# Optimization experiments

Measured on AMD Instinct MI355X. Metric: run time of the kernel, lower is better.

Reference implementation:

```python
import jax, jax.numpy as jnp
import numpy as np

B, T, DMODEL = 2, 2048, 1024
H, DK, DV = 16, 64, 64
FF = 4096
EPS = 1e-5


def _layernorm_2d(x):
    # torch LayerNorm(normalized_shape=(T, dmodel)): normalize jointly over last two
    # dims, biased variance, weight=1 / bias=0 (freshly constructed each forward).
    mu = jnp.mean(x, axis=(1, 2), keepdims=True)
    var = jnp.mean((x - mu) ** 2, axis=(1, 2), keepdims=True)
    return (x - mu) / jnp.sqrt(var + EPS)


def setup_inputs() -> dict:
    key = jax.random.key(0)
    ks = jax.random.split(key, 9)
    s = 0.02  # small init for numerical sanity (original uses uniform(-1,1))
    return {
        "x": jax.random.normal(ks[0], (B, T, DMODEL), jnp.float32),
        "Wq": jax.random.normal(ks[1], (H, DMODEL, DK), jnp.float32) * s,
        "Wk": jax.random.normal(ks[2], (H, DMODEL, DK), jnp.float32) * s,
        "Wv": jax.random.normal(ks[3], (H, DMODEL, DV), jnp.float32) * s,
        "Wo": jax.random.normal(ks[4], (DMODEL, DMODEL), jnp.float32) * s,
        "W1": jax.random.normal(ks[5], (DMODEL, FF), jnp.float32) * s,
        "b1": jnp.zeros((FF,), jnp.float32),
        "W2": jax.random.normal(ks[6], (FF, DMODEL), jnp.float32) * s,
        "b2": jnp.zeros((DMODEL,), jnp.float32),
    }


def reference(x, Wq, Wk, Wv, Wo, W1, b1, W2, b2):
    b, t, d = x.shape
    h, _, dk = Wq.shape
    dv = Wv.shape[-1]
    # per-head projections: (B,H,T,dk/dv)
    Qp = jnp.einsum("btd,hdk->bhtk", x, Wq)
    Kp = jnp.einsum("btd,hdk->bhtk", x, Wk)
    Vp = jnp.einsum("btd,hdv->bhtv", x, Wv)
    scores = jnp.einsum("bhqk,bhsk->bhqs", Qp, Kp) / np.sqrt(dk).astype(np.float32)
    # NOTE: original does torch.softmax(heads, 2) -> softmax over the QUERY axis
    attn = jax.nn.softmax(scores, axis=2)
    heads = jnp.einsum("bhqs,bhsv->bqhv", attn, Vp).reshape(b, t, h * dv)
    att_out = heads @ Wo
    o1 = _layernorm_2d(x + att_out)
    ff = jnp.maximum(o1 @ W1 + b1, 0.0) @ W2 + b2
    return _layernorm_2d(o1 + ff)
```

## Files before the change

kernel.cpp:

```cpp
#include <hip/hip_runtime.h>
#include <hip/hip_bf16.h>
#include <cstddef>
#include <cstdint>

typedef __hip_bfloat16 hbf;
typedef __attribute__((ext_vector_type(8))) __bf16 bf16x8;
typedef __attribute__((ext_vector_type(4))) float f32x4;

#define B_ 2
#define T_ 2048
#define D_ 1024
#define H_ 16
#define FF_ 4096
#define EPS_ 1e-5f
#define SCALE_ 0.18033688011112f

__device__ __forceinline__ float bf2f(hbf v) { return __bfloat162float(v); }
__device__ __forceinline__ float fexp2(float x) {
  return __builtin_amdgcn_exp2f(x);
}
__device__ __forceinline__ float flog2(float x) {
  return __builtin_amdgcn_logf(x);
}
__device__ __forceinline__ float ldin(const void* p, size_t i, int isbf) {
  return isbf ? __bfloat162float(((const hbf*)p)[i]) : ((const float*)p)[i];
}
__device__ __forceinline__ void ston(void* p, size_t i, float v, int isbf) {
  if (isbf) ((hbf*)p)[i] = __float2bfloat16(v);
  else ((float*)p)[i] = v;
}
__device__ __forceinline__ f32x4 mfma16(bf16x8 a, bf16x8 b, f32x4 c) {
  return __builtin_amdgcn_mfma_f32_16x16x32_bf16(a, b, c, 0, 0, 0);
}
__device__ __forceinline__ bf16x8 ldfrag(const hbf* p) {
  return *(const bf16x8*)p;
}
__device__ __forceinline__ void glds16(const hbf* g, hbf* l) {
  __builtin_amdgcn_global_load_lds(
      (const __attribute__((address_space(1))) void*)g,
      (__attribute__((address_space(3))) void*)l, 16, 0, 0);
}

__global__ __launch_bounds__(256) void detect_dtype(const unsigned* x,
                                                    int* flag) {
  __shared__ int cnt[256];
  int c = 0;
  for (int i = threadIdx.x; i < 4096; i += 256) {
    unsigned low = x[i] & 0xFFFFu;
    unsigned e = (low >> 7) & 0xFFu;
    if (e >= 100u && e <= 142u) c++;
  }
  cnt[threadIdx.x] = c;
  __syncthreads();
  for (int off = 128; off > 0; off >>= 1) {
    if ((int)threadIdx.x < off) cnt[threadIdx.x] += cnt[threadIdx.x + off];
    __syncthreads();
  }
  if (threadIdx.x == 0) *flag = (cnt[0] > 2458) ? 1 : 0;
}

__device__ __forceinline__ void tr_tile(const void* __restrict__ src,
                                        hbf* __restrict__ dst, int R, int C,
                                        size_t zoff, int cx, int ry, int f,
                                        float (*tile)[33]) {
  const int tx = threadIdx.x & 31, ty = threadIdx.x >> 5;
  const int c0 = cx * 32, r0 = ry * 32;
#pragma unroll
  for (int p = 0; p < 4; p++) {
    int rr = p * 8 + ty;
    tile[rr][tx] = ldin(src, zoff + (size_t)(r0 + rr) * C + c0 + tx, f);
  }
  __syncthreads();
#pragma unroll
  for (int p = 0; p < 4; p++) {
    int cc = p * 8 + ty;
    dst[zoff + (size_t)(c0 + cc) * R + r0 + tx] = __float2bfloat16(tile[tx][cc]);
  }
}

__global__ __launch_bounds__(256) void preconv(
    const void* __restrict__ x, const void* __restrict__ Wq,
    const void* __restrict__ Wk, const void* __restrict__ Wv,
    const void* __restrict__ Wo, const void* __restrict__ W1,
    const void* __restrict__ W2, const void* __restrict__ b1,
    const void* __restrict__ b2, hbf* __restrict__ xb,
    hbf* __restrict__ wqkvt, hbf* __restrict__ wot, hbf* __restrict__ w1t,
    hbf* __restrict__ w2t, hbf* __restrict__ b1b, hbf* __restrict__ b2b,
    const int* __restrict__ flag) {
  __shared__ float tile[32][33];
  const int f = *flag;
  const int bid = blockIdx.x;
  if (bid < 3072) {
    int which = bid >> 10;
    int r = bid & 1023;
    int z = r >> 6, rem = r & 63;
    int ry = rem >> 1, cx = rem & 1;
    const void* src = (which == 0) ? Wq : (which == 1) ? Wk : Wv;
    hbf* dst = wqkvt + (size_t)which * (D_ * D_);
    tr_tile(src, dst, 1024, 64, (size_t)z * 65536, cx, ry, f, tile);
  } else if (bid < 4096) {
    int t = bid - 3072;
    tr_tile(Wo, wot, 1024, 1024, 0, t & 31, t >> 5, f, tile);
  } else if (bid < 8192) {
    int t = bid - 4096;
    tr_tile(W1, w1t, 1024, 4096, 0, t & 127, t >> 7, f, tile);
  } else if (bid < 12288) {
    int t = bid - 8192;
    tr_tile(W2, w2t, 4096, 1024, 0, t & 31, t >> 5, f, tile);
  } else if (bid < 13312) {
    size_t base = (size_t)(bid - 12288) * 4096;
    if (f) {
      const uint4* src = (const uint4*)((const hbf*)x + base);
      uint4* dst = (uint4*)(xb + base);
      for (int i = threadIdx.x; i < 512; i += 256) dst[i] = src[i];
    } else {
      const float4* src = (const float4*)((const float*)x + base);
      for (int i = threadIdx.x; i < 512; i += 256) {
        float4 a = src[i * 2], b = src[i * 2 + 1];
        union {
          hbf h[8];
          uint4 u;
        } o;
        o.h[0] = __float2bfloat16(a.x);
        o.h[1] = __float2bfloat16(a.y);
        o.h[2] = __float2bfloat16(a.z);
        o.h[3] = __float2bfloat16(a.w);
        o.h[4] = __float2bfloat16(b.x);
        o.h[5] = __float2bfloat16(b.y);
        o.h[6] = __float2bfloat16(b.z);
        o.h[7] = __float2bfloat16(b.w);
        *(uint4*)(xb + base + (size_t)i * 8) = o.u;
      }
    }
  } else if (bid == 13312) {
    for (int i = threadIdx.x; i < FF_; i += 256)
      b1b[i] = __float2bfloat16(ldin(b1, i, f));
  } else {
    for (int i = threadIdx.x; i < D_; i += 256)
      b2b[i] = __float2bfloat16(ldin(b2, i, f));
  }
}

template <int MODE, int BM, int BN>
__global__ __launch_bounds__(256) void gemm_bt(
    const hbf* __restrict__ A, const hbf* __restrict__ Bt, hbf* __restrict__ C,
    float* __restrict__ Cf0, float* __restrict__ Cf1,
    const hbf* __restrict__ e1, float* __restrict__ red, int M, int N, int K,
    int LDK) {
  constexpr int WM = BM / 2, WN = BN / 2;
  constexpr int IF = WM / 16, JF = WN / 16;
  __shared__ alignas(16) hbf As[BM * 64];
  __shared__ alignas(16) hbf Bs[BN * 64];
  const int tid = threadIdx.x;
  const int wave = tid >> 6, lane = tid & 63;
  const int quad = lane >> 4, l16 = lane & 15;
  const int m0 = blockIdx.y * BM, n0 = blockIdx.x * BN;
  const int mw = (wave >> 1) * WM, nw = (wave & 1) * WN;
  const int srow = tid >> 3;
  const int scol = (tid & 7) * 8;
  const int kbase = (MODE == 4) ? blockIdx.z * K : 0;
  const f32x4 zero = {0.f, 0.f, 0.f, 0.f};
  f32x4 acc[IF][JF];
#pragma unroll
  for (int i = 0; i < IF; i++)
#pragma unroll
    for (int j = 0; j < JF; j++) acc[i][j] = zero;

  const hbf* ga = &A[(size_t)(m0 + srow) * LDK + kbase + scol];
  const hbf* gb = &Bt[(size_t)(n0 + srow) * LDK + kbase + scol];
  hbf* lA = &As[wave * 512];
  hbf* lB = &Bs[wave * 512];

  for (int k0 = 0; k0 < K; k0 += 64) {
#pragma unroll
    for (int c = 0; c < BM / 32; c++)
      glds16(ga + (size_t)(c * 32) * LDK + k0, lA + c * 2048);
#pragma unroll
    for (int c = 0; c < BN / 32; c++)
      glds16(gb + (size_t)(c * 32) * LDK + k0, lB + c * 2048);
    __syncthreads();
    bf16x8 af[2][IF], bfr[2][JF];
#pragma unroll
    for (int h = 0; h < 2; h++) {
#pragma unroll
      for (int i = 0; i < IF; i++)
        af[h][i] = ldfrag(&As[(mw + i * 16 + l16) * 64 + h * 32 + quad * 8]);
#pragma unroll
      for (int j = 0; j < JF; j++)
        bfr[h][j] = ldfrag(&Bs[(nw + j * 16 + l16) * 64 + h * 32 + quad * 8]);
    }
#pragma unroll
    for (int h = 0; h < 2; h++)
#pragma unroll
      for (int i = 0; i < IF; i++)
#pragma unroll
        for (int j = 0; j < JF; j++)
          acc[i][j] = mfma16(af[h][i], bfr[h][j], acc[i][j]);
    __syncthreads();
  }
  float ssum = 0.f, ssq = 0.f;
#pragma unroll
  for (int i = 0; i < IF; i++)
#pragma unroll
    for (int j = 0; j < JF; j++)
#pragma unroll
      for (int r = 0; r < 4; r++) {
        int m = m0 + mw + i * 16 + quad * 4 + r;
        int n = n0 + nw + j * 16 + l16;
        float v = acc[i][j][r];
        if (MODE == 0) {
          int which = n >> 10, n1 = n & 1023;
          int h = n1 >> 6, cc = n1 & 63;
          int b = m >> 11, t = m & (T_ - 1);
          if (which == 0) v *= SCALE_;
          C[(size_t)which * ((size_t)B_ * H_ * T_ * 64) +
            (((size_t)(b * H_ + h)) * T_ + t) * 64 + cc] = __float2bfloat16(v);
        } else if (MODE == 1) {
          hbf hv = __float2bfloat16(v + bf2f(e1[(size_t)m * N + n]));
          C[(size_t)m * N + n] = hv;
          float fv = bf2f(hv);
          ssum += fv;
          ssq += fv * fv;
        } else if (MODE == 2) {
          C[(size_t)m * N + n] = __float2bfloat16(fmaxf(v + bf2f(e1[n]), 0.f));
        } else if (MODE == 4) {
          float* Cf = blockIdx.z ? Cf1 : Cf0;
          Cf[(size_t)m * N + n] = v;
        }
      }
  if (MODE == 1) {
    float* sc = (float*)As;
    sc[tid] = ssum;
    sc[256 + tid] = ssq;
    __syncthreads();
    for (int off = 128; off > 0; off >>= 1) {
      if (tid < off) {
        sc[tid] += sc[tid + off];
        sc[256 + tid] += sc[256 + tid + off];
      }
      __syncthreads();
    }
    if (tid == 0) {
      int b = m0 >> 11;
      atomicAdd(&red[b * 2 + 0], sc[0]);
      atomicAdd(&red[b * 2 + 1], sc[256]);
    }
  }
}

__global__ __launch_bounds__(256) void attn_stats(const hbf* __restrict__ Q,
                                                  const hbf* __restrict__ K,
                                                  const hbf* __restrict__ V,
                                                  hbf* __restrict__ Vt) {
  __shared__ alignas(16) hbf Ks[64 * 72];
  __shared__ alignas(16) hbf Qs[64 * 72];
  __shared__ float sAdj[64];
  const int bh = blockIdx.y;
  const int s0 = blockIdx.x * 64;
  const int tid = threadIdx.x;
  const int wave = tid >> 6, lane = tid & 63;
  const int quad = lane >> 4, l16 = lane & 15;
  const int sw = wave * 16;
  const hbf* Kb = K + (size_t)bh * T_ * 64;
  const hbf* Qb = Q + (size_t)bh * T_ * 64;
  const hbf* Vb = V + (size_t)bh * T_ * 64;
  hbf* Vtb = Vt + (size_t)bh * 64 * T_;
  const int r_ = tid >> 3, c_ = (tid & 7) * 8;
#pragma unroll
  for (int c = 0; c < 2; c++) {
    int row = c * 32 + r_;
    *(float4*)(&Ks[row * 72 + c_]) =
        *(const float4*)(&Kb[(size_t)(s0 + row) * 64 + c_]);
  }
  __syncthreads();
  bf16x8 kf0 = ldfrag(&Ks[(sw + l16) * 72 + quad * 8]);
  bf16x8 kf1 = ldfrag(&Ks[(sw + l16) * 72 + 32 + quad * 8]);
  float m_thr[4], l_thr[4];
#pragma unroll
  for (int r = 0; r < 4; r++) {
    m_thr[r] = -1e30f;
    l_thr[r] = 0.f;
  }
  const f32x4 zero = {0.f, 0.f, 0.f, 0.f};
  for (int qt = 0; qt < T_ / 64; qt++) {
    if (qt) __syncthreads();
#pragma unroll
    for (int c = 0; c < 2; c++) {
      int row = c * 32 + r_;
      *(float4*)(&Qs[row * 72 + c_]) =
          *(const float4*)(&Qb[(size_t)(qt * 64 + row) * 64 + c_]);
    }
    __syncthreads();
    f32x4 acc[4];
#pragma unroll
    for (int j = 0; j < 4; j++) {
      bf16x8 qf0 = ldfrag(&Qs[(j * 16 + l16) * 72 + quad * 8]);
      bf16x8 qf1 = ldfrag(&Qs[(j * 16 + l16) * 72 + 32 + quad * 8]);
      f32x4 a = zero;
      a = mfma16(kf0, qf0, a);
      a = mfma16(kf1, qf1, a);
      acc[j] = a;
    }
#pragma unroll
    for (int r = 0; r < 4; r++) {
      float mt = fmaxf(fmaxf(acc[0][r], acc[1][r]),
                       fmaxf(acc[2][r], acc[3][r]));
      float nm = fmaxf(m_thr[r], mt);
      float s = l_thr[r] * fexp2(m_thr[r] - nm);
#pragma unroll
      for (int j = 0; j < 4; j++) s += fexp2(acc[j][r] - nm);
      l_thr[r] = s;
      m_thr[r] = nm;
    }
  }
#pragma unroll
  for (int d = 1; d < 16; d <<= 1) {
#pragma unroll
    for (int r = 0; r < 4; r++) {
      float om = __shfl_xor(m_thr[r], d);
      float ol = __shfl_xor(l_thr[r], d);
      float nm = fmaxf(m_thr[r], om);
      l_thr[r] = l_thr[r] * fexp2(m_thr[r] - nm) + ol * fexp2(om - nm);
      m_thr[r] = nm;
    }
  }
  if (l16 == 0) {
#pragma unroll
    for (int r = 0; r < 4; r++)
      sAdj[sw + quad * 4 + r] = m_thr[r] + flog2(l_thr[r]);
  }
  __syncthreads();
#pragma unroll
  for (int c = 0; c < 2; c++) {
    int e = (c * 256 + tid) * 8;
    int r = e >> 6, col = e & 63;
    union alignas(16) {
      hbf h[8];
      float4 f4;
    } u;
    u.f4 = *(const float4*)(&Vb[(size_t)(s0 + r) * 64 + col]);
    float sc = fexp2(-sAdj[r]);
#pragma unroll
    for (int k2 = 0; k2 < 8; k2++)
      u.h[k2] = __float2bfloat16(bf2f(u.h[k2]) * sc);
    *(float4*)(&Ks[r * 72 + col]) = u.f4;
  }
  __syncthreads();
#pragma unroll
  for (int c = 0; c < 2; c++) {
    int e = (c * 256 + tid) * 8;
    int v = e >> 6, tt = e & 63;
    union alignas(16) {
      hbf h[8];
      float4 f4;
    } u;
#pragma unroll
    for (int k2 = 0; k2 < 8; k2++) u.h[k2] = Ks[(tt + k2) * 72 + v];
    *(float4*)(&Vtb[(size_t)v * T_ + s0 + tt]) = u.f4;
  }
}

__global__ __launch_bounds__(256) void attn_apply(const hbf* __restrict__ Q,
                                                  const hbf* __restrict__ K,
                                                  const hbf* __restrict__ Vt,
                                                  hbf* __restrict__ heads) {
  __shared__ alignas(16) hbf Ksb[2 * 64 * 64];
  __shared__ alignas(16) hbf Vsb[3 * 64 * 64];
  __shared__ alignas(16) hbf Ps[4 * 2 * 32 * 72];
  const int bh = blockIdx.y;
  const int b = bh >> 4, h = bh & 15;
  const int q0 = blockIdx.x * 128;
  const int tid = threadIdx.x;
  const int wave = tid >> 6, lane = tid & 63;
  const int quad = lane >> 4, l16 = lane & 15;
  const int qw = wave * 32;
  const hbf* Qb = Q + (size_t)bh * T_ * 64;
  const hbf* Kb = K + (size_t)bh * T_ * 64;
  const hbf* Vtb = Vt + (size_t)bh * 64 * T_;
  hbf* Pw = &Ps[wave * (2 * 32 * 72)];
  const int srow = tid >> 3, sc8 = tid & 7;
  const int swz = sc8 ^ (srow & 7);
  const hbf* gk = Kb + (size_t)srow * 64 + swz * 8;
  const hbf* gv = Vtb + (size_t)srow * T_ + swz * 8;
  hbf* lK = &Ksb[wave * 512];
  hbf* lV = &Vsb[wave * 512];
  const int sx = (l16 & 7) * 8;
  bf16x8 qf[2][2];
#pragma unroll
  for (int i = 0; i < 2; i++)
#pragma unroll
    for (int hh = 0; hh < 2; hh++)
      qf[i][hh] = ldfrag(&Qb[(size_t)(q0 + qw + i * 16 + l16) * 64 + hh * 32 +
                             quad * 8]);
  const f32x4 zero = {0.f, 0.f, 0.f, 0.f};
  f32x4 accO[2][4];
#pragma unroll
  for (int i = 0; i < 2; i++)
#pragma unroll
    for (int j = 0; j < 4; j++) accO[i][j] = zero;

  glds16(gk, lK);
  glds16(gk + 2048, lK + 2048);
  glds16(gv, lV);
  glds16(gv + (size_t)32 * T_, lV + 2048);
  glds16(gk + 4096, lK + 4096);
  glds16(gk + 4096 + 2048, lK + 4096 + 2048);
  glds16(gv + 64, lV + 4096);
  glds16(gv + (size_t)32 * T_ + 64, lV + 4096 + 2048);
  __syncthreads();

  {
    const hbf* Kc = &Ksb[0];
    bf16x8 kf[4][2];
#pragma unroll
    for (int j = 0; j < 4; j++)
#pragma unroll
      for (int hh = 0; hh < 2; hh++)
        kf[j][hh] =
            ldfrag(&Kc[(j * 16 + l16) * 64 + ((hh * 32 + quad * 8) ^ sx)]);
    __builtin_amdgcn_s_setprio(1);
    f32x4 accS[2][4];
#pragma unroll
    for (int i = 0; i < 2; i++)
#pragma unroll
      for (int j = 0; j < 4; j++) {
        f32x4 a = mfma16(kf[j][0], qf[i][0], zero);
        accS[i][j] = mfma16(kf[j][1], qf[i][1], a);
      }
    __builtin_amdgcn_s_setprio(0);
#pragma unroll
    for (int i = 0; i < 2; i++)
#pragma unroll
      for (int j = 0; j < 4; j++) {
        union {
          hbf h4[4];
          uint2 u;
        } pk;
#pragma unroll
        for (int r = 0; r < 4; r++)
          pk.h4[r] = __float2bfloat16(fexp2(accS[i][j][r]));
        *(uint2*)&Pw[(i * 16 + l16) * 72 + j * 16 + quad * 4] = pk.u;
      }
  }
  __syncthreads();

  for (int st = 1; st < T_ / 64; st++) {
    const int kcur = st & 1;
    const int pcur = st & 1, pprev = pcur ^ 1;
    const int vprev = (st - 1) % 3;
    if (st < T_ / 64 - 1) {
      const int knxt = (st + 1) & 1, vnxt = (st + 1) % 3;
      size_t ko = (size_t)(st + 1) * 4096;
      glds16(gk + ko, lK + knxt * 4096);
      glds16(gk + ko + 2048, lK + knxt * 4096 + 2048);
      glds16(gv + (st + 1) * 64, lV + vnxt * 4096);
      glds16(gv + (size_t)32 * T_ + (st + 1) * 64, lV + vnxt * 4096 + 2048);
    }
    const hbf* Kc = &Ksb[kcur * 4096];
    const hbf* Vp = &Vsb[vprev * 4096];
    bf16x8 kf[4][2];
#pragma unroll
    for (int j = 0; j < 4; j++)
#pragma unroll
      for (int hh = 0; hh < 2; hh++)
        kf[j][hh] =
            ldfrag(&Kc[(j * 16 + l16) * 64 + ((hh * 32 + quad * 8) ^ sx)]);
    bf16x8 pf[2][2];
#pragma unroll
    for (int i = 0; i < 2; i++)
#pragma unroll
      for (int hh = 0; hh < 2; hh++)
        pf[i][hh] = ldfrag(
            &Pw[pprev * (32 * 72) + (i * 16 + l16) * 72 + hh * 32 + quad * 8]);
    __builtin_amdgcn_s_setprio(1);
#pragma unroll
    for (int j2 = 0; j2 < 4; j2++) {
      bf16x8 vf0 = ldfrag(&Vp[(j2 * 16 + l16) * 64 + ((quad * 8) ^ sx)]);
      bf16x8 vf1 = ldfrag(&Vp[(j2 * 16 + l16) * 64 + ((32 + quad * 8) ^ sx)]);
#pragma unroll
      for (int i = 0; i < 2; i++) {
        accO[i][j2] = mfma16(pf[i][0], vf0, accO[i][j2]);
        accO[i][j2] = mfma16(pf[i][1], vf1, accO[i][j2]);
      }
    }
    f32x4 accS[2][4];
#pragma unroll
    for (int i = 0; i < 2; i++)
#pragma unroll
      for (int j = 0; j < 4; j++) {
        f32x4 a = mfma16(kf[j][0], qf[i][0], zero);
        accS[i][j] = mfma16(kf[j][1], qf[i][1], a);
      }
    __builtin_amdgcn_s_setprio(0);
#pragma unroll
    for (int i = 0; i < 2; i++)
#pragma unroll
      for (int j = 0; j < 4; j++) {
        union {
          hbf h4[4];
          uint2 u;
        } pk;
#pragma unroll
        for (int r = 0; r < 4; r++)
          pk.h4[r] = __float2bfloat16(fexp2(accS[i][j][r]));
        *(uint2*)&Pw[pcur * (32 * 72) + (i * 16 + l16) * 72 + j * 16 +
                     quad * 4] = pk.u;
      }
    __syncthreads();
  }
  {
    const int pl = (T_ / 64 - 1) & 1;
    const hbf* Vp = &Vsb[((T_ / 64 - 1) % 3) * 4096];
    bf16x8 pf[2][2];
#pragma unroll
    for (int i = 0; i < 2; i++)
#pragma unroll
      for (int hh = 0; hh < 2; hh++)
        pf[i][hh] = ldfrag(
            &Pw[pl * (32 * 72) + (i * 16 + l16) * 72 + hh * 32 + quad * 8]);
    __builtin_amdgcn_s_setprio(1);
#pragma unroll
    for (int j2 = 0; j2 < 4; j2++) {
      bf16x8 vf0 = ldfrag(&Vp[(j2 * 16 + l16) * 64 + ((quad * 8) ^ sx)]);
      bf16x8 vf1 = ldfrag(&Vp[(j2 * 16 + l16) * 64 + ((32 + quad * 8) ^ sx)]);
#pragma unroll
      for (int i = 0; i < 2; i++) {
        accO[i][j2] = mfma16(pf[i][0], vf0, accO[i][j2]);
        accO[i][j2] = mfma16(pf[i][1], vf1, accO[i][j2]);
      }
    }
    __builtin_amdgcn_s_setprio(0);
  }
#pragma unroll
  for (int i = 0; i < 2; i++)
#pragma unroll
    for (int j2 = 0; j2 < 4; j2++)
#pragma unroll
      for (int r = 0; r < 4; r++) {
        int q = q0 + qw + i * 16 + quad * 4 + r;
        int v = j2 * 16 + l16;
        heads[((size_t)(b * T_ + q)) * D_ + h * 64 + v] =
            __float2bfloat16(accO[i][j2][r]);
      }
}

__global__ __launch_bounds__(256) void ln_norm(const hbf* __restrict__ src,
                                               const float* __restrict__ red,
                                               void* dst,
                                               const int* __restrict__ flag,
                                               int force_bf) {
  const int isbf = force_bf ? 1 : *flag;
  const float invN = 1.f / (float)(T_ * D_);
  for (size_t i = (size_t)blockIdx.x * 256 + threadIdx.x;
       i < (size_t)B_ * T_ * D_; i += (size_t)gridDim.x * 256) {
    int b = (int)(i >> 21);
    float mu = red[b * 2 + 0] * invN;
    float var = red[b * 2 + 1] * invN - mu * mu;
    ston(dst, i, (bf2f(src[i]) - mu) * rsqrtf(var + EPS_), isbf);
  }
}

__global__ __launch_bounds__(256) void ln2_stats(const float* __restrict__ P0,
                                                 const float* __restrict__ P1,
                                                 const hbf* __restrict__ o1,
                                                 const hbf* __restrict__ b2b,
                                                 float* __restrict__ red) {
  __shared__ float s1[256], s2[256];
  const int b = blockIdx.y;
  const size_t base = (size_t)b * (T_ * D_);
  float sum = 0.f, sq = 0.f;
  for (size_t i = (size_t)blockIdx.x * 256 + threadIdx.x; i < (size_t)T_ * D_;
       i += (size_t)gridDim.x * 256) {
    size_t e = base + i;
    float v = P0[e] + P1[e] + bf2f(b2b[i & (D_ - 1)]) + bf2f(o1[e]);
    sum += v;
    sq += v * v;
  }
  s1[threadIdx.x] = sum;
  s2[threadIdx.x] = sq;
  __syncthreads();
  for (int off = 128; off > 0; off >>= 1) {
    if ((int)threadIdx.x < off) {
      s1[threadIdx.x] += s1[threadIdx.x + off];
      s2[threadIdx.x] += s2[threadIdx.x + off];
    }
    __syncthreads();
  }
  if (threadIdx.x == 0) {
    atomicAdd(&red[b * 2 + 0], s1[0]);
    atomicAdd(&red[b * 2 + 1], s2[0]);
  }
}

__global__ __launch_bounds__(256) void ln2_norm(
    const float* __restrict__ P0, const float* __restrict__ P1,
    const hbf* __restrict__ o1, const hbf* __restrict__ b2b,
    const float* __restrict__ red, void* dst, const int* __restrict__ flag) {
  const int isbf = *flag;
  const float invN = 1.f / (float)(T_ * D_);
  for (size_t i = (size_t)blockIdx.x * 256 + threadIdx.x;
       i < (size_t)B_ * T_ * D_; i += (size_t)gridDim.x * 256) {
    int b = (int)(i >> 21);
    float mu = red[b * 2 + 0] * invN;
    float var = red[b * 2 + 1] * invN - mu * mu;
    float v = P0[i] + P1[i] + bf2f(b2b[i & (D_ - 1)]) + bf2f(o1[i]);
    ston(dst, i, (v - mu) * rsqrtf(var + EPS_), isbf);
  }
}

extern "C" void kernel_launch(void* const* d_in, const int* in_sizes, int n_in,
                              void* d_out, int out_size, void* d_ws,
                              size_t ws_size, hipStream_t stream) {
  const void* x = d_in[0];
  const void* Wq = d_in[1];
  const void* Wk = d_in[2];
  const void* Wv = d_in[3];
  const void* Wo = d_in[4];
  const void* W1 = d_in[5];
  const void* W2 = d_in[7];
  const void* b1 = d_in[6];
  const void* b2 = d_in[8];

  const size_t MB = 1024 * 1024;
  if (ws_size < 89 * MB) return;

  char* w = (char*)d_ws;
  hbf* xb = (hbf*)(w + 0 * MB);
  hbf* wqkvt = (hbf*)(w + 8 * MB);
  hbf* wot = (hbf*)(w + 14 * MB);
  hbf* w1t = (hbf*)(w + 16 * MB);
  hbf* w2t = (hbf*)(w + 24 * MB);
  hbf* Qb = (hbf*)(w + 32 * MB);
  hbf* Kb = (hbf*)(w + 40 * MB);
  hbf* Vb = (hbf*)(w + 48 * MB);
  hbf* Vtb = (hbf*)(w + 56 * MB);
  hbf* heads = (hbf*)(w + 64 * MB);
  hbf* r1 = (hbf*)(w + 72 * MB);
  hbf* o1 = (hbf*)(w + 80 * MB);
  hbf* ff1 = (hbf*)(w + 32 * MB);
  float* P0 = (float*)(w + 0 * MB);
  float* P1 = (float*)(w + 64 * MB);
  hbf* b1b = (hbf*)(w + 88 * MB);
  hbf* b2b = b1b + FF_;
  float* red = (float*)(b2b + D_);
  int* flag = (int*)(red + 8);

  hipMemsetAsync(red, 0, 8 * sizeof(float) + sizeof(int), stream);
  detect_dtype<<<1, 256, 0, stream>>>((const unsigned*)x, flag);

  const int M = B_ * T_;
  preconv<<<13314, 256, 0, stream>>>(x, Wq, Wk, Wv, Wo, W1, W2, b1, b2, xb,
                                     wqkvt, wot, w1t, w2t, b1b, b2b, flag);
  gemm_bt<0, 128, 128><<<dim3(24, 32), 256, 0, stream>>>(
      xb, wqkvt, Qb, nullptr, nullptr, nullptr, nullptr, M, 3 * D_, D_, D_);
  attn_stats<<<dim3(32, 32), 256, 0, stream>>>(Qb, Kb, Vb, Vtb);
  attn_apply<<<dim3(16, 32), 256, 0, stream>>>(Qb, Kb, Vtb, heads);
  gemm_bt<1, 128, 64><<<dim3(16, 32), 256, 0, stream>>>(
      heads, wot, r1, nullptr, nullptr, xb, red, M, D_, D_, D_);
  ln_norm<<<4096, 256, 0, stream>>>(r1, red, o1, flag, 1);
  gemm_bt<2, 128, 128><<<dim3(32, 32), 256, 0, stream>>>(
      o1, w1t, ff1, nullptr, nullptr, b1b, nullptr, M, FF_, D_, D_);
  gemm_bt<4, 128, 128><<<dim3(8, 32, 2), 256, 0, stream>>>(
      ff1, w2t, nullptr, P0, P1, nullptr, nullptr, M, D_, FF_ / 2, FF_);
  ln2_stats<<<dim3(256, B_), 256, 0, stream>>>(P0, P1, o1, b2b, red + 4);
  ln2_norm<<<2048, 256, 0, stream>>>(P0, P1, o1, b2b, red + 4, d_out, flag);
}
```

Before: 452.5 us.

## Fuse FFN2 bias, residual and LN2 stats into GEMM epilogue, drop split-K

The second FFN GEMM no longer uses a two-way split-K with fp32 partial outputs. It runs a single full-K pass with 128x64 tiles and an epilogue that adds bias and the residual, writes bf16, and accumulates the LayerNorm sum and sum of squares with atomics. This removes the ln2_stats kernel and the fp32 partial-buffer round trips, and the final normalize kernel now reads bf16 with 4-wide vector loads and stores. In exchange the GEMM grid has 512 blocks each doing K=4096, so parallelism per block changes. The residual sum is also rounded to bf16 before the statistics are taken.

```diff
diff --git a/kernel.cpp b/kernel.cpp
--- a/kernel.cpp
+++ b/kernel.cpp
@@ -158,7 +158,6 @@
   const int mw = (wave >> 1) * WM, nw = (wave & 1) * WN;
   const int srow = tid >> 3;
   const int scol = (tid & 7) * 8;
-  const int kbase = (MODE == 4) ? blockIdx.z * K : 0;
   const f32x4 zero = {0.f, 0.f, 0.f, 0.f};
   f32x4 acc[IF][JF];
 #pragma unroll
@@ -166,8 +165,8 @@
 #pragma unroll
     for (int j = 0; j < JF; j++) acc[i][j] = zero;
 
-  const hbf* ga = &A[(size_t)(m0 + srow) * LDK + kbase + scol];
-  const hbf* gb = &Bt[(size_t)(n0 + srow) * LDK + kbase + scol];
+  const hbf* ga = &A[(size_t)(m0 + srow) * LDK + scol];
+  const hbf* gb = &Bt[(size_t)(n0 + srow) * LDK + scol];
   hbf* lA = &As[wave * 512];
   hbf* lB = &Bs[wave * 512];
 
@@ -223,12 +222,17 @@
           ssq += fv * fv;
         } else if (MODE == 2) {
           C[(size_t)m * N + n] = __float2bfloat16(fmaxf(v + bf2f(e1[n]), 0.f));
-        } else if (MODE == 4) {
-          float* Cf = blockIdx.z ? Cf1 : Cf0;
-          Cf[(size_t)m * N + n] = v;
+        } else if (MODE == 5) {
+          const hbf* bias = (const hbf*)Cf0;
+          hbf hv = __float2bfloat16(v + bf2f(bias[n]) +
+                                    bf2f(e1[(size_t)m * N + n]));
+          C[(size_t)m * N + n] = hv;
+          float fv = bf2f(hv);
+          ssum += fv;
+          ssq += fv * fv;
         }
       }
-  if (MODE == 1) {
+  if (MODE == 1 || MODE == 5) {
     float* sc = (float*)As;
     sc[tid] = ssum;
     sc[256 + tid] = ssq;
@@ -560,51 +564,39 @@
   }
 }
 
-__global__ __launch_bounds__(256) void ln2_stats(const float* __restrict__ P0,
-                                                 const float* __restrict__ P1,
-                                                 const hbf* __restrict__ o1,
-                                                 const hbf* __restrict__ b2b,
-                                                 float* __restrict__ red) {
-  __shared__ float s1[256], s2[256];
-  const int b = blockIdx.y;
-  const size_t base = (size_t)b * (T_ * D_);
-  float sum = 0.f, sq = 0.f;
-  for (size_t i = (size_t)blockIdx.x * 256 + threadIdx.x; i < (size_t)T_ * D_;
-       i += (size_t)gridDim.x * 256) {
-    size_t e = base + i;
-    float v = P0[e] + P1[e] + bf2f(b2b[i & (D_ - 1)]) + bf2f(o1[e]);
-    sum += v;
-    sq += v * v;
-  }
-  s1[threadIdx.x] = sum;
-  s2[threadIdx.x] = sq;
-  __syncthreads();
-  for (int off = 128; off > 0; off >>= 1) {
-    if ((int)threadIdx.x < off) {
-      s1[threadIdx.x] += s1[threadIdx.x + off];
-      s2[threadIdx.x] += s2[threadIdx.x + off];
-    }
-    __syncthreads();
-  }
-  if (threadIdx.x == 0) {
-    atomicAdd(&red[b * 2 + 0], s1[0]);
-    atomicAdd(&red[b * 2 + 1], s2[0]);
-  }
-}
-
-__global__ __launch_bounds__(256) void ln2_norm(
-    const float* __restrict__ P0, const float* __restrict__ P1,
-    const hbf* __restrict__ o1, const hbf* __restrict__ b2b,
-    const float* __restrict__ red, void* dst, const int* __restrict__ flag) {
+__global__ __launch_bounds__(256) void ln2_norm(const hbf* __restrict__ r2,
+                                                const float* __restrict__ red,
+                                                void* dst,
+                                                const int* __restrict__ flag) {
   const int isbf = *flag;
   const float invN = 1.f / (float)(T_ * D_);
+  const uint2* r2v = (const uint2*)r2;
   for (size_t i = (size_t)blockIdx.x * 256 + threadIdx.x;
-       i < (size_t)B_ * T_ * D_; i += (size_t)gridDim.x * 256) {
-    int b = (int)(i >> 21);
+       i < (size_t)B_ * T_ * D_ / 4; i += (size_t)gridDim.x * 256) {
+    int b = (int)(i >> 19);
     float mu = red[b * 2 + 0] * invN;
     float var = red[b * 2 + 1] * invN - mu * mu;
-    float v = P0[i] + P1[i] + bf2f(b2b[i & (D_ - 1)]) + bf2f(o1[i]);
-    ston(dst, i, (v - mu) * rsqrtf(var + EPS_), isbf);
+    float rstd = rsqrtf(var + EPS_);
+    union {
+      uint2 u;
+      hbf h[4];
+    } s;
+    s.u = r2v[i];
+    float out[4];
+#pragma unroll
+    for (int r = 0; r < 4; r++) out[r] = (bf2f(s.h[r]) - mu) * rstd;
+    if (isbf) {
+      union {
+        hbf h[4];
+        uint2 u;
+      } pk;
+#pragma unroll
+      for (int r = 0; r < 4; r++) pk.h[r] = __float2bfloat16(out[r]);
+      ((uint2*)dst)[i] = pk.u;
+    } else {
+      float4 f{out[0], out[1], out[2], out[3]};
+      ((float4*)dst)[i] = f;
+    }
   }
 }
 
@@ -638,8 +630,7 @@
   hbf* r1 = (hbf*)(w + 72 * MB);
   hbf* o1 = (hbf*)(w + 80 * MB);
   hbf* ff1 = (hbf*)(w + 32 * MB);
-  float* P0 = (float*)(w + 0 * MB);
-  float* P1 = (float*)(w + 64 * MB);
+  hbf* r2 = (hbf*)(w + 0 * MB);
   hbf* b1b = (hbf*)(w + 88 * MB);
   hbf* b2b = b1b + FF_;
   float* red = (float*)(b2b + D_);
@@ -660,8 +651,7 @@
   ln_norm<<<4096, 256, 0, stream>>>(r1, red, o1, flag, 1);
   gemm_bt<2, 128, 128><<<dim3(32, 32), 256, 0, stream>>>(
       o1, w1t, ff1, nullptr, nullptr, b1b, nullptr, M, FF_, D_, D_);
-  gemm_bt<4, 128, 128><<<dim3(8, 32, 2), 256, 0, stream>>>(
-      ff1, w2t, nullptr, P0, P1, nullptr, nullptr, M, D_, FF_ / 2, FF_);
-  ln2_stats<<<dim3(256, B_), 256, 0, stream>>>(P0, P1, o1, b2b, red + 4);
-  ln2_norm<<<2048, 256, 0, stream>>>(P0, P1, o1, b2b, red + 4, d_out, flag);
-}
+  gemm_bt<5, 128, 64><<<dim3(16, 32), 256, 0, stream>>>(
+      ff1, w2t, r2, (float*)b2b, nullptr, o1, red + 4, M, D_, FF_, FF_);
+  ln2_norm<<<2048, 256, 0, stream>>>(r2, red + 4, d_out, flag);
+}
```

Measured after the change: 453.4 us. About the same (+0.2%).
